# Kernel tuning notes

Hardware: AMD Instinct MI355X
Metric: run time of the kernel (lower is better)

Reference implementation:

```python
import jax, jax.numpy as jnp
import numpy as np

N = 65536   # num nodes
E = N * 16  # num edges (avg degree 16)
D = 64      # in_feats = h_feats = out_feats


def _lin(key, din, dout):
    # torch.nn.Linear default init: U(-1/sqrt(din), 1/sqrt(din))
    s = 1.0 / np.sqrt(din)
    kw, kb = jax.random.split(key)
    W = jax.random.uniform(kw, (din, dout), jnp.float32, -s, s)
    b = jax.random.uniform(kb, (dout,), jnp.float32, -s, s)
    return W, b


def setup_inputs() -> dict:
    key = jax.random.key(0)
    ks = jax.random.split(key, 8)
    x = jax.random.normal(ks[0], (N, D), jnp.float32)
    edge_index = jax.random.randint(ks[1], (2, E), 0, N, dtype=jnp.int32)
    # Each SAGEConv: out = lin_l(mean_agg(x_src -> dst)) + lin_r(x)
    # lin_l has bias, lin_r has no bias (PyG SAGEConv defaults)
    w_l1, b1 = _lin(ks[2], D, D)
    w_r1, _ = _lin(ks[3], D, D)
    w_l2, b2 = _lin(ks[4], D, D)
    w_r2, _ = _lin(ks[5], D, D)
    w_l3, b3 = _lin(ks[6], D, D)
    w_r3, _ = _lin(ks[7], D, D)
    return {"x": x, "edge_index": edge_index,
            "w_l1": w_l1, "b1": b1, "w_r1": w_r1,
            "w_l2": w_l2, "b2": b2, "w_r2": w_r2,
            "w_l3": w_l3, "b3": b3, "w_r3": w_r3}


def _sage_conv(x, src, dst, inv_deg, W_l, b, W_r):
    # mean-aggregate source features at destination nodes, then linear + root term
    n = x.shape[0]
    agg = jax.ops.segment_sum(x[src], dst, num_segments=n)  # [N, D]
    agg = agg * inv_deg
    return agg @ W_l + b + x @ W_r


def reference(x, edge_index, w_l1, b1, w_r1, w_l2, b2, w_r2, w_l3, b3, w_r3):
    src, dst = edge_index[0], edge_index[1]
    n = x.shape[0]
    deg = jax.ops.segment_sum(jnp.ones((src.shape[0],), x.dtype), dst,
                              num_segments=n)
    inv_deg = (1.0 / jnp.maximum(deg, 1.0))[:, None]  # [N, 1]
    h = jax.nn.relu(_sage_conv(x, src, dst, inv_deg, w_l1, b1, w_r1))
    h = jax.nn.relu(_sage_conv(h, src, dst, inv_deg, w_l2, b2, w_r2))
    out = _sage_conv(h, src, dst, inv_deg, w_l3, b3, w_r3)
    return out
```

## Files before the change

kernel.cpp:

```cpp
#include <hip/hip_runtime.h>

constexpr int D     = 64;
constexpr int PCAP  = 32;
constexpr int CAP   = 64;
constexpr int NBUCK = 256;
constexpr int BNODE = 256;
constexpr int NBINA = 256;
constexpr int SCAP  = 48;

typedef __attribute__((ext_vector_type(8))) short          bf16x8;
typedef __attribute__((ext_vector_type(4))) float          f32x4;
typedef __attribute__((ext_vector_type(8))) unsigned short ushort8;
typedef __attribute__((ext_vector_type(4))) unsigned short ushort4v;
typedef __attribute__((ext_vector_type(4))) int            i32x4;

__device__ __forceinline__ unsigned short f2bf(float f) {
    unsigned int u = __float_as_uint(f);
    u += 0x7FFFu + ((u >> 16) & 1u);
    return (unsigned short)(u >> 16);
}
__device__ __forceinline__ void acc4(float& x, float& y, float& z, float& w, uint2 r) {
    x += __uint_as_float(r.x << 16); y += __uint_as_float(r.x & 0xffff0000u);
    z += __uint_as_float(r.y << 16); w += __uint_as_float(r.y & 0xffff0000u);
}

__global__ __launch_bounds__(256) void mega_kernel(
    const int* __restrict__ src, const int* __restrict__ dst, int E4,
    unsigned* __restrict__ binned, int* __restrict__ cnts,
    const float4* __restrict__ xin, ushort4v* __restrict__ xb, int n4, int nbConv,
    const float* __restrict__ wl1, const float* __restrict__ wr1,
    const float* __restrict__ wl2, const float* __restrict__ wr2,
    const float* __restrict__ wl3, const float* __restrict__ wr3,
    unsigned short* __restrict__ WhAll)
{
    const int tid = threadIdx.x;
    if ((int)blockIdx.x < NBINA) {
        __shared__ int cur[NBUCK];
        cur[tid] = 0;
        __syncthreads();
        const int per = E4 / NBINA;
        const int t0 = blockIdx.x * per;
        const int te = t0 + per;
        for (int it = t0 + tid; it < te; it += 256) {
            const i32x4 dv = *(((const i32x4*)dst) + it);
            const i32x4 sv = *(((const i32x4*)src) + it);
            #pragma unroll
            for (int j = 0; j < 4; ++j) {
                const int b = (unsigned)dv[j] >> 8;
                const int p = atomicAdd(&cur[b], 1);
                if (p < SCAP)
                    binned[((size_t)b * NBINA + blockIdx.x) * SCAP + p] =
                        ((unsigned)sv[j] & 0xffffu) | (((unsigned)dv[j] & 255u) << 16);
            }
        }
        __syncthreads();
        cnts[tid * NBINA + blockIdx.x] = min(cur[tid], SCAP);
        return;
    }
    if ((int)blockIdx.x < NBINA + nbConv) {
        const int t = ((int)blockIdx.x - NBINA) * 256 + tid;
        if (t < n4) {
            const float4 v = xin[t];
            ushort4v o;
            o[0] = f2bf(v.x); o[1] = f2bf(v.y); o[2] = f2bf(v.z); o[3] = f2bf(v.w);
            xb[t] = o;
        }
        return;
    }
    const int pb = (int)blockIdx.x - NBINA - nbConv;
    const int layer = pb >> 2;
    const float* Wl = (layer == 0) ? wl1 : (layer == 1) ? wl2 : wl3;
    const float* Wr = (layer == 0) ? wr1 : (layer == 1) ? wr2 : wr3;
    unsigned short* Wh = WhAll + layer * D * 128;
    const int p = (pb & 3) * 256 + tid;
    const int col = p >> 4, kc = p & 15;
    ushort8 hi;
    #pragma unroll
    for (int j = 0; j < 8; ++j) {
        const int k = kc * 8 + j;
        const float f = (k < 64) ? Wl[k * 64 + col] : Wr[(k - 64) * 64 + col];
        hi[j] = (short)f2bf(f);
    }
    *reinterpret_cast<ushort8*>(&Wh[col * 128 + kc * 8]) = hi;
}

__global__ __launch_bounds__(256) void binB_kernel(
    const unsigned* __restrict__ binned, const int* __restrict__ cnts,
    unsigned short* __restrict__ prim, unsigned short* __restrict__ ovfl,
    int* __restrict__ cursor)
{
    __shared__ int cnt[BNODE];
    const int tid = threadIdx.x;
    const int b = blockIdx.x;
    cnt[tid] = 0;
    __syncthreads();
    const int c = cnts[b * NBINA + tid];
    const unsigned* cell = binned + ((size_t)b * NBINA + tid) * SCAP;
    for (int p = 0; p < c; ++p) {
        const unsigned e = cell[p];
        const int nl = (e >> 16) & 255;
        const unsigned short s = (unsigned short)(e & 0xffffu);
        const int q = atomicAdd(&cnt[nl], 1);
        const int node = b * BNODE + nl;
        if (q < PCAP)      prim[node * PCAP + q]          = s;
        else if (q < CAP)  ovfl[node * PCAP + (q - PCAP)] = s;
    }
    __syncthreads();
    cursor[b * BNODE + tid] = cnt[tid];
}

__global__ __launch_bounds__(256) void gather_b(
    const unsigned short* __restrict__ tab, const unsigned short* __restrict__ prim,
    const unsigned short* __restrict__ ovfl, const int* __restrict__ cursor,
    unsigned short* __restrict__ aggb, int n)
{
    const int wave = threadIdx.x >> 6;
    const int lane = threadIdx.x & 63;
    const int g = lane >> 4;
    const int i = lane & 15;
    const int nodeA = blockIdx.x * 8 + wave * 2;
    const int nodeB = nodeA + 1;
    const int half = lane >> 5;
    const int slot = lane & 31;
    const int myNode = half ? nodeB : nodeA;
    int raw = prim[myNode * PCAP + slot];
    const int cA = cursor[nodeA];
    const int cB = cursor[nodeB];
    const int dA = min(cA, CAP), dB = min(cB, CAP);
    const int lim = half ? dB : dA;
    raw = (slot < lim) ? raw : 0;
    const int maxd = max(dA, dB);

    float a0=0.f,a1=0.f,a2=0.f,a3=0.f;
    float b0=0.f,b1=0.f,b2=0.f,b3=0.f;

    auto step = [&](int r, int l0, int s0) {
        const int nA0 = __shfl(r, l0),      nA1 = __shfl(r, l0 + 4);
        const int nA2 = __shfl(r, l0 + 8),  nA3 = __shfl(r, l0 + 12);
        const int nB0 = __shfl(r, 32 + l0),     nB1 = __shfl(r, 32 + l0 + 4);
        const int nB2 = __shfl(r, 32 + l0 + 8), nB3 = __shfl(r, 32 + l0 + 12);
        const uint2 rA0 = *reinterpret_cast<const uint2*>(tab + (size_t)nA0 * D + i * 4);
        const uint2 rA1 = *reinterpret_cast<const uint2*>(tab + (size_t)nA1 * D + i * 4);
        const uint2 rA2 = *reinterpret_cast<const uint2*>(tab + (size_t)nA2 * D + i * 4);
        const uint2 rA3 = *reinterpret_cast<const uint2*>(tab + (size_t)nA3 * D + i * 4);
        const uint2 rB0 = *reinterpret_cast<const uint2*>(tab + (size_t)nB0 * D + i * 4);
        const uint2 rB1 = *reinterpret_cast<const uint2*>(tab + (size_t)nB1 * D + i * 4);
        const uint2 rB2 = *reinterpret_cast<const uint2*>(tab + (size_t)nB2 * D + i * 4);
        const uint2 rB3 = *reinterpret_cast<const uint2*>(tab + (size_t)nB3 * D + i * 4);
        if (s0      < dA) acc4(a0, a1, a2, a3, rA0);
        if (s0 + 4  < dA) acc4(a0, a1, a2, a3, rA1);
        if (s0 + 8  < dA) acc4(a0, a1, a2, a3, rA2);
        if (s0 + 12 < dA) acc4(a0, a1, a2, a3, rA3);
        if (s0      < dB) acc4(b0, b1, b2, b3, rB0);
        if (s0 + 4  < dB) acc4(b0, b1, b2, b3, rB1);
        if (s0 + 8  < dB) acc4(b0, b1, b2, b3, rB2);
        if (s0 + 12 < dB) acc4(b0, b1, b2, b3, rB3);
    };

    step(raw, g, g);
    step(raw, 16 + g, 16 + g);
    if (maxd > PCAP) {
        int ov = ovfl[myNode * PCAP + slot];
        ov = (PCAP + slot < lim) ? ov : 0;
        step(ov, g, 32 + g);
        if (maxd > 48) step(ov, 16 + g, 48 + g);
    }

    a0 += __shfl_xor(a0, 16); a1 += __shfl_xor(a1, 16);
    a2 += __shfl_xor(a2, 16); a3 += __shfl_xor(a3, 16);
    a0 += __shfl_xor(a0, 32); a1 += __shfl_xor(a1, 32);
    a2 += __shfl_xor(a2, 32); a3 += __shfl_xor(a3, 32);
    b0 += __shfl_xor(b0, 16); b1 += __shfl_xor(b1, 16);
    b2 += __shfl_xor(b2, 16); b3 += __shfl_xor(b3, 16);
    b0 += __shfl_xor(b0, 32); b1 += __shfl_xor(b1, 32);
    b2 += __shfl_xor(b2, 32); b3 += __shfl_xor(b3, 32);
    if (g == 0) {
        const float inv = 1.0f / fmaxf((float)cA, 1.0f);
        ushort4v o;
        o[0] = f2bf(a0 * inv); o[1] = f2bf(a1 * inv);
        o[2] = f2bf(a2 * inv); o[3] = f2bf(a3 * inv);
        *reinterpret_cast<ushort4v*>(aggb + (size_t)nodeA * D + i * 4) = o;
    } else if (g == 1) {
        const float inv = 1.0f / fmaxf((float)cB, 1.0f);
        ushort4v o;
        o[0] = f2bf(b0 * inv); o[1] = f2bf(b1 * inv);
        o[2] = f2bf(b2 * inv); o[3] = f2bf(b3 * inv);
        *reinterpret_cast<ushort4v*>(aggb + (size_t)nodeB * D + i * 4) = o;
    }
}

template<bool RELU, bool BF16OUT>
__global__ __launch_bounds__(256) void gemm_mfma(
    const unsigned short* __restrict__ aggb, const unsigned short* __restrict__ root,
    const unsigned short* __restrict__ Wh,
    const float* __restrict__ bias, unsigned short* outb, float* outf)
{
    __shared__ unsigned short Ah[64 * 128];
    __shared__ unsigned short Bh[64 * 128];
    const int tid = threadIdx.x;
    const int node0 = blockIdx.x * 64;

    #pragma unroll
    for (int i = 0; i < 4; ++i) {
        const int p = i * 256 + tid;
        const int col = p >> 4, kc = p & 15;
        const int dst = col * 128 + ((kc ^ (col & 7)) << 3);
        *reinterpret_cast<ushort8*>(&Bh[dst]) =
            *reinterpret_cast<const ushort8*>(Wh + col * 128 + kc * 8);
    }
    #pragma unroll
    for (int i = 0; i < 4; ++i) {
        const int p = i * 256 + tid;
        const int node = p >> 4, kc = p & 15;
        const unsigned short* s = (kc < 8)
            ? aggb + (size_t)(node0 + node) * 64 + kc * 8
            : root + (size_t)(node0 + node) * 64 + (kc - 8) * 8;
        const int dst = node * 128 + ((kc ^ (node & 7)) << 3);
        *reinterpret_cast<ushort8*>(&Ah[dst]) =
            *reinterpret_cast<const ushort8*>(s);
    }
    __syncthreads();

    const int lane = tid & 63, w = tid >> 6;
    const int rl = lane & 15, g = lane >> 4;
    const int arow = w * 16 + rl;

    f32x4 acc[4];
    #pragma unroll
    for (int t = 0; t < 4; ++t) {
        const float b = bias[t * 16 + rl];
        acc[t] = (f32x4){b, b, b, b};
    }
    #pragma unroll
    for (int kc4 = 0; kc4 < 4; ++kc4) {
        const int c = kc4 * 4 + g;
        const int aoff = arow * 128 + ((c ^ (arow & 7)) << 3);
        const bf16x8 ah = *reinterpret_cast<const bf16x8*>(&Ah[aoff]);
        #pragma unroll
        for (int t = 0; t < 4; ++t) {
            const int bcol = t * 16 + rl;
            const int boff = bcol * 128 + ((c ^ (bcol & 7)) << 3);
            const bf16x8 bh = *reinterpret_cast<const bf16x8*>(&Bh[boff]);
            acc[t] = __builtin_amdgcn_mfma_f32_16x16x32_bf16(ah, bh, acc[t], 0, 0, 0);
        }
    }
    #pragma unroll
    for (int t = 0; t < 4; ++t) {
        #pragma unroll
        for (int r = 0; r < 4; ++r) {
            float v = acc[t][r];
            if (RELU) v = fmaxf(v, 0.0f);
            const size_t off = (size_t)(node0 + w * 16 + g * 4 + r) * 64 + t * 16 + rl;
            if (BF16OUT) outb[off] = f2bf(v);
            else         outf[off] = v;
        }
    }
}

extern "C" void kernel_launch(void* const* d_in, const int* in_sizes, int n_in,
                              void* d_out, int out_size, void* d_ws, size_t ws_size,
                              hipStream_t stream)
{
    const float* x    = (const float*)d_in[0];
    const int*   ei   = (const int*)d_in[1];
    const int    E    = in_sizes[1] / 2;
    const int*   src  = ei;
    const int*   dstp = ei + E;
    const float* wl1 = (const float*)d_in[2];
    const float* b1  = (const float*)d_in[3];
    const float* wr1 = (const float*)d_in[4];
    const float* wl2 = (const float*)d_in[5];
    const float* b2  = (const float*)d_in[6];
    const float* wr2 = (const float*)d_in[7];
    const float* wl3 = (const float*)d_in[8];
    const float* b3  = (const float*)d_in[9];
    const float* wr3 = (const float*)d_in[10];
    float* out = (float*)d_out;
    const int n = in_sizes[0] / D;

    unsigned short* prim = (unsigned short*)d_ws;
    unsigned short* ovfl = prim + (size_t)n * PCAP;
    int*   cursor = (int*)(ovfl + (size_t)n * PCAP);
    int*   cnts   = cursor + n;
    unsigned short* Wh  = (unsigned short*)(cnts + NBUCK * NBINA);
    unsigned short* aggb = Wh + 3 * D * 128;
    unsigned* binned = (unsigned*)aggb;
    unsigned short* hb2 = aggb + (size_t)n * D;

    unsigned short* xb  = (unsigned short*)d_out;
    unsigned short* hb1 = xb + (size_t)n * D;

    const int E4 = E / 4;
    const int nbConv = (n * 16) / 256;

    mega_kernel<<<NBINA + nbConv + 12, 256, 0, stream>>>(
        src, dstp, E4, binned, cnts,
        (const float4*)x, (ushort4v*)xb, n * 16, nbConv,
        wl1, wr1, wl2, wr2, wl3, wr3, Wh);
    binB_kernel<<<NBUCK, 256, 0, stream>>>(binned, cnts, prim, ovfl, cursor);

    const int gatherBlocks = n / 8;
    const int gemmBlocks   = n / 64;

    gather_b<<<gatherBlocks, 256, 0, stream>>>(xb, prim, ovfl, cursor, aggb, n);
    gemm_mfma<true, true><<<gemmBlocks, 256, 0, stream>>>(
        aggb, xb, Wh, b1, hb1, nullptr);

    gather_b<<<gatherBlocks, 256, 0, stream>>>(hb1, prim, ovfl, cursor, aggb, n);
    gemm_mfma<true, true><<<gemmBlocks, 256, 0, stream>>>(
        aggb, hb1, Wh + D * 128, b2, hb2, nullptr);

    gather_b<<<gatherBlocks, 256, 0, stream>>>(hb2, prim, ovfl, cursor, aggb, n);
    gemm_mfma<false, false><<<gemmBlocks, 256, 0, stream>>>(
        aggb, hb2, Wh + 2 * D * 128, b3, nullptr, out);
}
```

Before: 109.7 us.

## Fuse neighbor gather and MFMA GEMM into one per-layer kernel via LDS

```diff
diff --git a/kernel.cpp b/kernel.cpp
--- a/kernel.cpp
+++ b/kernel.cpp
@@ -109,151 +109,137 @@
     cursor[b * BNODE + tid] = cnt[tid];
 }
 
-__global__ __launch_bounds__(256) void gather_b(
-    const unsigned short* __restrict__ tab, const unsigned short* __restrict__ prim,
-    const unsigned short* __restrict__ ovfl, const int* __restrict__ cursor,
-    unsigned short* __restrict__ aggb, int n)
-{
-    const int wave = threadIdx.x >> 6;
-    const int lane = threadIdx.x & 63;
-    const int g = lane >> 4;
-    const int i = lane & 15;
-    const int nodeA = blockIdx.x * 8 + wave * 2;
-    const int nodeB = nodeA + 1;
-    const int half = lane >> 5;
-    const int slot = lane & 31;
-    const int myNode = half ? nodeB : nodeA;
-    int raw = prim[myNode * PCAP + slot];
-    const int cA = cursor[nodeA];
-    const int cB = cursor[nodeB];
-    const int dA = min(cA, CAP), dB = min(cB, CAP);
-    const int lim = half ? dB : dA;
-    raw = (slot < lim) ? raw : 0;
-    const int maxd = max(dA, dB);
-
-    float a0=0.f,a1=0.f,a2=0.f,a3=0.f;
-    float b0=0.f,b1=0.f,b2=0.f,b3=0.f;
-
-    auto step = [&](int r, int l0, int s0) {
-        const int nA0 = __shfl(r, l0),      nA1 = __shfl(r, l0 + 4);
-        const int nA2 = __shfl(r, l0 + 8),  nA3 = __shfl(r, l0 + 12);
-        const int nB0 = __shfl(r, 32 + l0),     nB1 = __shfl(r, 32 + l0 + 4);
-        const int nB2 = __shfl(r, 32 + l0 + 8), nB3 = __shfl(r, 32 + l0 + 12);
-        const uint2 rA0 = *reinterpret_cast<const uint2*>(tab + (size_t)nA0 * D + i * 4);
-        const uint2 rA1 = *reinterpret_cast<const uint2*>(tab + (size_t)nA1 * D + i * 4);
-        const uint2 rA2 = *reinterpret_cast<const uint2*>(tab + (size_t)nA2 * D + i * 4);
-        const uint2 rA3 = *reinterpret_cast<const uint2*>(tab + (size_t)nA3 * D + i * 4);
-        const uint2 rB0 = *reinterpret_cast<const uint2*>(tab + (size_t)nB0 * D + i * 4);
-        const uint2 rB1 = *reinterpret_cast<const uint2*>(tab + (size_t)nB1 * D + i * 4);
-        const uint2 rB2 = *reinterpret_cast<const uint2*>(tab + (size_t)nB2 * D + i * 4);
-        const uint2 rB3 = *reinterpret_cast<const uint2*>(tab + (size_t)nB3 * D + i * 4);
-        if (s0      < dA) acc4(a0, a1, a2, a3, rA0);
-        if (s0 + 4  < dA) acc4(a0, a1, a2, a3, rA1);
-        if (s0 + 8  < dA) acc4(a0, a1, a2, a3, rA2);
-        if (s0 + 12 < dA) acc4(a0, a1, a2, a3, rA3);
-        if (s0      < dB) acc4(b0, b1, b2, b3, rB0);
-        if (s0 + 4  < dB) acc4(b0, b1, b2, b3, rB1);
-        if (s0 + 8  < dB) acc4(b0, b1, b2, b3, rB2);
-        if (s0 + 12 < dB) acc4(b0, b1, b2, b3, rB3);
-    };
-
-    step(raw, g, g);
-    step(raw, 16 + g, 16 + g);
-    if (maxd > PCAP) {
-        int ov = ovfl[myNode * PCAP + slot];
-        ov = (PCAP + slot < lim) ? ov : 0;
-        step(ov, g, 32 + g);
-        if (maxd > 48) step(ov, 16 + g, 48 + g);
-    }
-
-    a0 += __shfl_xor(a0, 16); a1 += __shfl_xor(a1, 16);
-    a2 += __shfl_xor(a2, 16); a3 += __shfl_xor(a3, 16);
-    a0 += __shfl_xor(a0, 32); a1 += __shfl_xor(a1, 32);
-    a2 += __shfl_xor(a2, 32); a3 += __shfl_xor(a3, 32);
-    b0 += __shfl_xor(b0, 16); b1 += __shfl_xor(b1, 16);
-    b2 += __shfl_xor(b2, 16); b3 += __shfl_xor(b3, 16);
-    b0 += __shfl_xor(b0, 32); b1 += __shfl_xor(b1, 32);
-    b2 += __shfl_xor(b2, 32); b3 += __shfl_xor(b3, 32);
-    if (g == 0) {
-        const float inv = 1.0f / fmaxf((float)cA, 1.0f);
-        ushort4v o;
-        o[0] = f2bf(a0 * inv); o[1] = f2bf(a1 * inv);
-        o[2] = f2bf(a2 * inv); o[3] = f2bf(a3 * inv);
-        *reinterpret_cast<ushort4v*>(aggb + (size_t)nodeA * D + i * 4) = o;
-    } else if (g == 1) {
-        const float inv = 1.0f / fmaxf((float)cB, 1.0f);
-        ushort4v o;
-        o[0] = f2bf(b0 * inv); o[1] = f2bf(b1 * inv);
-        o[2] = f2bf(b2 * inv); o[3] = f2bf(b3 * inv);
-        *reinterpret_cast<ushort4v*>(aggb + (size_t)nodeB * D + i * 4) = o;
-    }
-}
-
 template<bool RELU, bool BF16OUT>
-__global__ __launch_bounds__(256) void gemm_mfma(
-    const unsigned short* __restrict__ aggb, const unsigned short* __restrict__ root,
-    const unsigned short* __restrict__ Wh,
-    const float* __restrict__ bias, unsigned short* outb, float* outf)
+__global__ __launch_bounds__(1024) void fused_layer(
+    const unsigned short* __restrict__ tab,
+    const unsigned short* __restrict__ prim, const unsigned short* __restrict__ ovfl,
+    const int* __restrict__ cursor,
+    const unsigned short* __restrict__ Wh, const float* __restrict__ bias,
+    unsigned short* outb, float* outf)
 {
     __shared__ unsigned short Ah[64 * 128];
     __shared__ unsigned short Bh[64 * 128];
     const int tid = threadIdx.x;
     const int node0 = blockIdx.x * 64;
-
-    #pragma unroll
-    for (int i = 0; i < 4; ++i) {
-        const int p = i * 256 + tid;
-        const int col = p >> 4, kc = p & 15;
+    const int wave = tid >> 6;
+    const int lane = tid & 63;
+    const int g = lane >> 4;
+    const int i = lane & 15;
+
+    {
+        const int col = tid >> 4, kc = tid & 15;
         const int dst = col * 128 + ((kc ^ (col & 7)) << 3);
         *reinterpret_cast<ushort8*>(&Bh[dst]) =
             *reinterpret_cast<const ushort8*>(Wh + col * 128 + kc * 8);
     }
-    #pragma unroll
-    for (int i = 0; i < 4; ++i) {
-        const int p = i * 256 + tid;
-        const int node = p >> 4, kc = p & 15;
-        const unsigned short* s = (kc < 8)
-            ? aggb + (size_t)(node0 + node) * 64 + kc * 8
-            : root + (size_t)(node0 + node) * 64 + (kc - 8) * 8;
-        const int dst = node * 128 + ((kc ^ (node & 7)) << 3);
+    if (tid < 512) {
+        const int ln = tid >> 3, kc8 = tid & 7;
+        const int kc = 8 + kc8;
+        const int dst = ln * 128 + ((kc ^ (ln & 7)) << 3);
         *reinterpret_cast<ushort8*>(&Ah[dst]) =
-            *reinterpret_cast<const ushort8*>(s);
+            *reinterpret_cast<const ushort8*>(tab + (size_t)(node0 + ln) * 64 + kc8 * 8);
+    }
+
+    const int half = lane >> 5;
+    const int slot = lane & 31;
+    for (int rnd = 0; rnd < 2; ++rnd) {
+        const int nodeA = node0 + wave * 4 + rnd * 2;
+        const int nodeB = nodeA + 1;
+        const int myNode = half ? nodeB : nodeA;
+        int raw = prim[myNode * PCAP + slot];
+        const int cA = cursor[nodeA];
+        const int cB = cursor[nodeB];
+        const int dA = min(cA, CAP), dB = min(cB, CAP);
+        const int lim = half ? dB : dA;
+        raw = (slot < lim) ? raw : 0;
+        const int maxd = max(dA, dB);
+
+        float a0 = 0.f, a1 = 0.f, a2 = 0.f, a3 = 0.f;
+        float b0 = 0.f, b1 = 0.f, b2 = 0.f, b3 = 0.f;
+        auto step = [&](int r, int l0, int s0) {
+            const int nA0 = __shfl(r, l0),      nA1 = __shfl(r, l0 + 4);
+            const int nA2 = __shfl(r, l0 + 8),  nA3 = __shfl(r, l0 + 12);
+            const int nB0 = __shfl(r, 32 + l0),     nB1 = __shfl(r, 32 + l0 + 4);
+            const int nB2 = __shfl(r, 32 + l0 + 8), nB3 = __shfl(r, 32 + l0 + 12);
+            const uint2 rA0 = *reinterpret_cast<const uint2*>(tab + (size_t)nA0 * D + i * 4);
+            const uint2 rA1 = *reinterpret_cast<const uint2*>(tab + (size_t)nA1 * D + i * 4);
+            const uint2 rA2 = *reinterpret_cast<const uint2*>(tab + (size_t)nA2 * D + i * 4);
+            const uint2 rA3 = *reinterpret_cast<const uint2*>(tab + (size_t)nA3 * D + i * 4);
+            const uint2 rB0 = *reinterpret_cast<const uint2*>(tab + (size_t)nB0 * D + i * 4);
+            const uint2 rB1 = *reinterpret_cast<const uint2*>(tab + (size_t)nB1 * D + i * 4);
+            const uint2 rB2 = *reinterpret_cast<const uint2*>(tab + (size_t)nB2 * D + i * 4);
+            const uint2 rB3 = *reinterpret_cast<const uint2*>(tab + (size_t)nB3 * D + i * 4);
+            if (s0      < dA) acc4(a0, a1, a2, a3, rA0);
+            if (s0 + 4  < dA) acc4(a0, a1, a2, a3, rA1);
+            if (s0 + 8  < dA) acc4(a0, a1, a2, a3, rA2);
+            if (s0 + 12 < dA) acc4(a0, a1, a2, a3, rA3);
+            if (s0      < dB) acc4(b0, b1, b2, b3, rB0);
+            if (s0 + 4  < dB) acc4(b0, b1, b2, b3, rB1);
+            if (s0 + 8  < dB) acc4(b0, b1, b2, b3, rB2);
+            if (s0 + 12 < dB) acc4(b0, b1, b2, b3, rB3);
+        };
+        step(raw, g, g);
+        step(raw, 16 + g, 16 + g);
+        if (maxd > PCAP) {
+            int ov = ovfl[myNode * PCAP + slot];
+            ov = (PCAP + slot < lim) ? ov : 0;
+            step(ov, g, 32 + g);
+            if (maxd > 48) step(ov, 16 + g, 48 + g);
+        }
+
+        a0 += __shfl_xor(a0, 16); a1 += __shfl_xor(a1, 16);
+        a2 += __shfl_xor(a2, 16); a3 += __shfl_xor(a3, 16);
+        a0 += __shfl_xor(a0, 32); a1 += __shfl_xor(a1, 32);
+        a2 += __shfl_xor(a2, 32); a3 += __shfl_xor(a3, 32);
+        b0 += __shfl_xor(b0, 16); b1 += __shfl_xor(b1, 16);
+        b2 += __shfl_xor(b2, 16); b3 += __shfl_xor(b3, 16);
+        b0 += __shfl_xor(b0, 32); b1 += __shfl_xor(b1, 32);
+        b2 += __shfl_xor(b2, 32); b3 += __shfl_xor(b3, 32);
+
+        const int kc = i >> 1;
+        if (g == 0) {
+            const float inv = 1.0f / fmaxf((float)cA, 1.0f);
+            const int ln = nodeA - node0;
+            const int dst = ln * 128 + ((kc ^ (ln & 7)) << 3) + (i & 1) * 4;
+            ushort4v o;
+            o[0] = f2bf(a0 * inv); o[1] = f2bf(a1 * inv);
+            o[2] = f2bf(a2 * inv); o[3] = f2bf(a3 * inv);
+            *reinterpret_cast<ushort4v*>(&Ah[dst]) = o;
+        } else if (g == 1) {
+            const float inv = 1.0f / fmaxf((float)cB, 1.0f);
+            const int ln = nodeB - node0;
+            const int dst = ln * 128 + ((kc ^ (ln & 7)) << 3) + (i & 1) * 4;
+            ushort4v o;
+            o[0] = f2bf(b0 * inv); o[1] = f2bf(b1 * inv);
+            o[2] = f2bf(b2 * inv); o[3] = f2bf(b3 * inv);
+            *reinterpret_cast<ushort4v*>(&Ah[dst]) = o;
+        }
     }
     __syncthreads();
 
-    const int lane = tid & 63, w = tid >> 6;
-    const int rl = lane & 15, g = lane >> 4;
-    const int arow = w * 16 + rl;
-
-    f32x4 acc[4];
-    #pragma unroll
-    for (int t = 0; t < 4; ++t) {
-        const float b = bias[t * 16 + rl];
-        acc[t] = (f32x4){b, b, b, b};
-    }
+    const int r0 = (wave >> 2) * 16;
+    const int c0 = (wave & 3) * 16;
+    const int rl = lane & 15;
+    const float bia = bias[c0 + rl];
+    f32x4 acc = (f32x4){bia, bia, bia, bia};
     #pragma unroll
     for (int kc4 = 0; kc4 < 4; ++kc4) {
         const int c = kc4 * 4 + g;
+        const int arow = r0 + rl;
         const int aoff = arow * 128 + ((c ^ (arow & 7)) << 3);
         const bf16x8 ah = *reinterpret_cast<const bf16x8*>(&Ah[aoff]);
-        #pragma unroll
-        for (int t = 0; t < 4; ++t) {
-            const int bcol = t * 16 + rl;
-            const int boff = bcol * 128 + ((c ^ (bcol & 7)) << 3);
-            const bf16x8 bh = *reinterpret_cast<const bf16x8*>(&Bh[boff]);
-            acc[t] = __builtin_amdgcn_mfma_f32_16x16x32_bf16(ah, bh, acc[t], 0, 0, 0);
-        }
+        const int bcol = c0 + rl;
+        const int boff = bcol * 128 + ((c ^ (bcol & 7)) << 3);
+        const bf16x8 bh = *reinterpret_cast<const bf16x8*>(&Bh[boff]);
+        acc = __builtin_amdgcn_mfma_f32_16x16x32_bf16(ah, bh, acc, 0, 0, 0);
     }
     #pragma unroll
-    for (int t = 0; t < 4; ++t) {
-        #pragma unroll
-        for (int r = 0; r < 4; ++r) {
-            float v = acc[t][r];
-            if (RELU) v = fmaxf(v, 0.0f);
-            const size_t off = (size_t)(node0 + w * 16 + g * 4 + r) * 64 + t * 16 + rl;
-            if (BF16OUT) outb[off] = f2bf(v);
-            else         outf[off] = v;
-        }
+    for (int r = 0; r < 4; ++r) {
+        float v = acc[r];
+        if (RELU) v = fmaxf(v, 0.0f);
+        const size_t off = (size_t)(node0 + r0 + g * 4 + r) * 64 + c0 + rl;
+        if (BF16OUT) outb[off] = f2bf(v);
+        else         outf[off] = v;
     }
 }
 
@@ -283,9 +269,9 @@
     int*   cursor = (int*)(ovfl + (size_t)n * PCAP);
     int*   cnts   = cursor + n;
     unsigned short* Wh  = (unsigned short*)(cnts + NBUCK * NBINA);
-    unsigned short* aggb = Wh + 3 * D * 128;
-    unsigned* binned = (unsigned*)aggb;
-    unsigned short* hb2 = aggb + (size_t)n * D;
+    unsigned short* unionArea = Wh + 3 * D * 128;
+    unsigned* binned = (unsigned*)unionArea;
+    unsigned short* hb2 = unionArea + (size_t)n * D;
 
     unsigned short* xb  = (unsigned short*)d_out;
     unsigned short* hb1 = xb + (size_t)n * D;
@@ -299,18 +285,12 @@
         wl1, wr1, wl2, wr2, wl3, wr3, Wh);
     binB_kernel<<<NBUCK, 256, 0, stream>>>(binned, cnts, prim, ovfl, cursor);
 
-    const int gatherBlocks = n / 8;
-    const int gemmBlocks   = n / 64;
-
-    gather_b<<<gatherBlocks, 256, 0, stream>>>(xb, prim, ovfl, cursor, aggb, n);
-    gemm_mfma<true, true><<<gemmBlocks, 256, 0, stream>>>(
-        aggb, xb, Wh, b1, hb1, nullptr);
-
-    gather_b<<<gatherBlocks, 256, 0, stream>>>(hb1, prim, ovfl, cursor, aggb, n);
-    gemm_mfma<true, true><<<gemmBlocks, 256, 0, stream>>>(
-        aggb, hb1, Wh + D * 128, b2, hb2, nullptr);
-
-    gather_b<<<gatherBlocks, 256, 0, stream>>>(hb2, prim, ovfl, cursor, aggb, n);
-    gemm_mfma<false, false><<<gemmBlocks, 256, 0, stream>>>(
-        aggb, hb2, Wh + 2 * D * 128, b3, nullptr, out);
-}
+    const int blocks = n / 64;
+
+    fused_layer<true, true><<<blocks, 1024, 0, stream>>>(
+        xb, prim, ovfl, cursor, Wh, b1, hb1, nullptr);
+    fused_layer<true, true><<<blocks, 1024, 0, stream>>>(
+        hb1, prim, ovfl, cursor, Wh + D * 128, b2, hb2, nullptr);
+    fused_layer<false, false><<<blocks, 1024, 0, stream>>>(
+        hb2, prim, ovfl, cursor, Wh + 2 * D * 128, b3, nullptr, out);
+}
```

After: 124.6 us. 13.6% more time.
